# Optimization experiments

Hardware: AMD Instinct MI355X
Metric: run time of the kernel (lower is better)

## Reference

```python
import jax, jax.numpy as jnp
import numpy as np

N_EMBD = 1024
N_HEAD = 16
HEAD_DIM = N_EMBD // N_HEAD


def setup_inputs() -> dict:
    key = jax.random.key(0)
    k1, k2, k3, k4, k5 = jax.random.split(key, 5)
    x = jax.random.normal(k1, (4, 2048, N_EMBD), dtype=jnp.float32)
    s_in = 1.0 / np.sqrt(N_EMBD)
    W_attn = jax.random.normal(k2, (N_EMBD, 3 * N_EMBD), dtype=jnp.float32) * s_in
    b_attn = jax.random.normal(k3, (3 * N_EMBD,), dtype=jnp.float32) * 0.01
    W_proj = jax.random.normal(k4, (N_EMBD, N_EMBD), dtype=jnp.float32) * s_in
    b_proj = jax.random.normal(k5, (N_EMBD,), dtype=jnp.float32) * 0.01
    return {"x": x, "W_attn": W_attn, "b_attn": b_attn, "W_proj": W_proj, "b_proj": b_proj}


def reference(x, W_attn, b_attn, W_proj, b_proj):
    B, T, C = x.shape
    qkv = jnp.einsum('btc,cd->btd', x, W_attn) + b_attn  # [B,T,3C]
    q, k, v = jnp.split(qkv, 3, axis=2)
    # [B,T,C] -> [B,H,T,Dh]
    def heads(t):
        return t.reshape(B, T, N_HEAD, HEAD_DIM).transpose(0, 2, 1, 3)
    q, k, v = heads(q), heads(k), heads(v)
    scale = HEAD_DIM ** -0.5
    att = jnp.einsum('bhqd,bhkd->bhqk', q, k) * scale  # [B,H,T,T]
    causal = jnp.tril(jnp.ones((T, T), dtype=bool))
    att = jnp.where(causal[None, None], att, -jnp.inf)
    att = jax.nn.softmax(att, axis=-1)
    y = jnp.einsum('bhqk,bhkd->bhqd', att, v)  # [B,H,T,Dh]
    y = y.transpose(0, 2, 1, 3).reshape(B, T, C)
    y = jnp.einsum('btc,cd->btd', y, W_proj) + b_proj
    return y
```

## Files before the change

kernel.cpp:

```cpp
#include <hip/hip_runtime.h>

typedef unsigned short u16;
typedef unsigned int u32;
typedef __bf16 bf16x8 __attribute__((ext_vector_type(8)));
typedef u16 u16x8 __attribute__((ext_vector_type(8)));
typedef u16 u16x4 __attribute__((ext_vector_type(4)));
typedef float f32x4 __attribute__((ext_vector_type(4)));
typedef float f32x16 __attribute__((ext_vector_type(16)));

#define BHTD 8388608
#define QSCALE 0.18033688f
#define SMAX 16.0f

__device__ __forceinline__ u16 f2bf(float f) {
  union { float f; u32 u; } x; x.f = f;
  u32 r = (x.u + 0x7FFFu + ((x.u >> 16) & 1u)) >> 16;
  return (u16)r;
}

__device__ __forceinline__ u32 cvt_pk_bf16(float lo, float hi) {
  u32 r;
  asm("v_cvt_pk_bf16_f32 %0, %1, %2" : "=v"(r) : "v"(lo), "v"(hi));
  return r;
}

__device__ __forceinline__ void permlane32_swap(u32& x, u32& y) {
  asm("v_permlane32_swap_b32 %0, %1" : "+v"(x), "+v"(y));
}

__device__ __forceinline__ void async_copy16(const u16* gsrc, u16* ldst) {
  __builtin_amdgcn_global_load_lds(
      (const __attribute__((address_space(1))) void*)gsrc,
      (__attribute__((address_space(3))) void*)ldst, 16, 0, 0);
}

__global__ __launch_bounds__(256) void conv_x_kernel(const float4* __restrict__ in,
                                                     u16x4* __restrict__ out, int n4) {
  int i = blockIdx.x * 256 + threadIdx.x;
  int stride = gridDim.x * 256;
  for (; i < n4; i += stride) {
    float4 v = in[i];
    u16x4 o = { f2bf(v.x), f2bf(v.y), f2bf(v.z), f2bf(v.w) };
    out[i] = o;
  }
}

__global__ __launch_bounds__(256) void transpose_bf16(const float* __restrict__ W,
                                                      u16* __restrict__ Wt, int K, int N) {
  __shared__ float t[64][65];
  int c0 = blockIdx.x * 64;
  int r0 = blockIdx.y * 64;
  int c = threadIdx.x & 63;
  int r4 = threadIdx.x >> 6;
#pragma unroll
  for (int j = 0; j < 16; ++j) {
    int r = j * 4 + r4;
    t[r][c] = W[(size_t)(r0 + r) * N + (c0 + c)];
  }
  __syncthreads();
#pragma unroll
  for (int j = 0; j < 16; ++j) {
    int n = j * 4 + r4;
    Wt[(size_t)(c0 + n) * K + (r0 + c)] = f2bf(t[c][n]);
  }
}

template <int MODE>
__global__ __launch_bounds__(256) void gemm_bf16(const u16* __restrict__ A,
                                                 const u16* __restrict__ Bt,
                                                 const float* __restrict__ bias,
                                                 float* __restrict__ outp,
                                                 u16* __restrict__ qkv, int grid_n) {
  __shared__ __attribute__((aligned(16))) u16 A_lds[128 * 64];
  __shared__ __attribute__((aligned(16))) u16 B_lds[128 * 64];
  const int tid = threadIdx.x;
  const int lane = tid & 63, wave = tid >> 6;
  const int wr = wave >> 1, wc = wave & 1;
  const int bn = blockIdx.x % grid_n, bm = blockIdx.x / grid_n;
  const int m0 = bm * 128, n0 = bn * 128;
  const int g = lane >> 4, c16 = lane & 15;
  const int lrow = lane >> 3, lslot = lane & 7;

  f32x4 acc[4][4] = {};

  for (int kt = 0; kt < 16; ++kt) {
#pragma unroll
    for (int i = 0; i < 4; ++i) {
      int mloc = (wave * 4 + i) * 8 + lrow;
      int col = kt * 64 + ((lslot ^ (mloc & 7)) << 3);
      async_copy16(&A[(size_t)(m0 + mloc) * 1024 + col], &A_lds[(wave * 4 + i) * 512]);
      async_copy16(&Bt[(size_t)(n0 + mloc) * 1024 + col], &B_lds[(wave * 4 + i) * 512]);
    }
    __syncthreads();
#pragma unroll
    for (int kk = 0; kk < 2; ++kk) {
      bf16x8 af[4], bfr[4];
#pragma unroll
      for (int mb = 0; mb < 4; ++mb) {
        int row = wr * 64 + mb * 16 + c16;
        int slot = (kk * 4 + g) ^ (row & 7);
        af[mb] = *(const bf16x8*)&A_lds[row * 64 + slot * 8];
        int rowb = wc * 64 + mb * 16 + c16;
        int slotb = (kk * 4 + g) ^ (rowb & 7);
        bfr[mb] = *(const bf16x8*)&B_lds[rowb * 64 + slotb * 8];
      }
#pragma unroll
      for (int mb = 0; mb < 4; ++mb)
#pragma unroll
        for (int nb = 0; nb < 4; ++nb)
          acc[mb][nb] = __builtin_amdgcn_mfma_f32_16x16x32_bf16(af[mb], bfr[nb], acc[mb][nb], 0, 0, 0);
    }
    __syncthreads();
  }

  float bv[4];
#pragma unroll
  for (int nb = 0; nb < 4; ++nb) bv[nb] = bias[n0 + wc * 64 + nb * 16 + c16];

#pragma unroll
  for (int mb = 0; mb < 4; ++mb) {
    int row0 = m0 + wr * 64 + mb * 16 + g * 4;
#pragma unroll
    for (int nb = 0; nb < 4; ++nb) {
      int col = n0 + wc * 64 + nb * 16 + c16;
      float bvn = bv[nb];
      if (MODE == 0) {
        int sel = col >> 10, ci = col & 1023;
        int hh = ci >> 6, d = ci & 63;
        int bb = row0 >> 11, t0 = row0 & 2047;
        float qs = (sel == 0) ? QSCALE : 1.0f;
        if (sel == 2) {
          u16x4 pk;
#pragma unroll
          for (int r = 0; r < 4; ++r) pk[r] = f2bf(acc[mb][nb][r] + bvn);
          *(u16x4*)&qkv[(size_t)2 * BHTD + (((size_t)(bb * 16 + hh) * 64 + d) << 11) + t0] = pk;
        } else {
#pragma unroll
          for (int r = 0; r < 4; ++r) {
            qkv[(size_t)sel * BHTD + (((size_t)(bb * 16 + hh) * 2048 + t0 + r) << 6) + d] =
                f2bf((acc[mb][nb][r] + bvn) * qs);
          }
        }
      } else {
#pragma unroll
        for (int r = 0; r < 4; ++r)
          outp[((size_t)(row0 + r) << 10) + col] = acc[mb][nb][r] + bvn;
      }
    }
  }
}

__global__ __launch_bounds__(512, 4) void attn_fwd(const u16* __restrict__ Q,
                                                   const u16* __restrict__ K,
                                                   const u16* __restrict__ VT,
                                                   u16* __restrict__ Y) {
  __shared__ __attribute__((aligned(16))) u16 Kl[2][2][64 * 64];
  __shared__ __attribute__((aligned(16))) u16 Vl[2][2][64 * 64];
  float* Pl = (float*)&Kl[0][0][0];
  float* Ll = (float*)&Vl[0][0][0];
  const float NEG_BIG = -1e30f;

  int bid = blockIdx.x;
  int p = bid >> 6, hd = bid & 63;
  size_t hb = (size_t)hd * (2048 * 64);
  const u16* Qh = Q + hb;
  const u16* Kh = K + hb;
  const u16* Vh = VT + hb;
  int tid = threadIdx.x, lane = tid & 63, w = tid >> 6;
  int rg = w & 3, par = w >> 2;
  int c32 = lane & 31, h = lane >> 5;
  const int xs = c32 & 7;

  int srow = tid >> 3;
  int swz = ((tid & 7) ^ (srow & 7)) << 3;

  for (int pass = 0; pass < 2; ++pass) {
    const int t128 = pass ? p : (15 - p);
    const int iters = t128 + 1;
    const int qrow = t128 * 128 + rg * 32 + c32;

    bf16x8 qf[4];
#pragma unroll
    for (int dk = 0; dk < 4; ++dk)
      qf[dk] = *(const bf16x8*)&Qh[(size_t)qrow * 64 + dk * 16 + 8 * h];

    async_copy16(&Kh[(size_t)srow * 64 + swz], &Kl[0][0][tid << 3]);
    async_copy16(&Kh[(size_t)(64 + srow) * 64 + swz], &Kl[0][1][tid << 3]);
    async_copy16(&Vh[(size_t)srow * 2048 + swz], &Vl[0][0][tid << 3]);
    async_copy16(&Vh[(size_t)srow * 2048 + 64 + swz], &Vl[0][1][tid << 3]);

    float l = 0.f;
    f32x16 o0 = {}, o1 = {};

    for (int it = 0; it < iters; ++it) {
      int cb = it & 1;
      __syncthreads();

      if (it + 1 < iters) {
        int kve = (it + 1) << 7, kvo = kve + 64;
        async_copy16(&Kh[(size_t)(kve + srow) * 64 + swz], &Kl[cb ^ 1][0][tid << 3]);
        async_copy16(&Kh[(size_t)(kvo + srow) * 64 + swz], &Kl[cb ^ 1][1][tid << 3]);
        async_copy16(&Vh[(size_t)srow * 2048 + kve + swz], &Vl[cb ^ 1][0][tid << 3]);
        async_copy16(&Vh[(size_t)srow * 2048 + kvo + swz], &Vl[cb ^ 1][1][tid << 3]);
      }

      const bool lastit = (it + 1 == iters);
      if (par && lastit && rg < 2) continue;
      const int kv0 = (2 * it + par) << 6;
      const bool mask = lastit && ((par == 0) == (rg < 2));

      bf16x8 kf[2][4];
#pragma unroll
      for (int kb = 0; kb < 2; ++kb)
#pragma unroll
        for (int dk = 0; dk < 4; ++dk)
          kf[kb][dk] =
              *(const bf16x8*)&Kl[cb][par][(kb * 32 + c32) * 64 + (((2 * dk + h) ^ xs) << 3)];
      f32x16 s0, s1;
#pragma unroll
      for (int i = 0; i < 16; ++i) { s0[i] = -SMAX; s1[i] = -SMAX; }
      __builtin_amdgcn_s_setprio(1);
#pragma unroll
      for (int dk = 0; dk < 4; ++dk) {
        s0 = __builtin_amdgcn_mfma_f32_32x32x16_bf16(kf[0][dk], qf[dk], s0, 0, 0, 0);
        s1 = __builtin_amdgcn_mfma_f32_32x32x16_bf16(kf[1][dk], qf[dk], s1, 0, 0, 0);
      }
      __builtin_amdgcn_s_setprio(0);

      if (mask) {
        int kvb = kv0 + 4 * h;
#pragma unroll
        for (int reg = 0; reg < 16; ++reg) {
          int kvl = kvb + 8 * (reg >> 2) + (reg & 3);
          if (kvl > qrow) s0[reg] = NEG_BIG;
          if (kvl + 32 > qrow) s1[reg] = NEG_BIG;
        }
      }

#pragma unroll
      for (int i = 0; i < 16; ++i) s0[i] = __builtin_exp2f(s0[i]);
#pragma unroll
      for (int i = 0; i < 16; ++i) s1[i] = __builtin_exp2f(s1[i]);
      float b0 = s0[0] + s1[0], b1 = s0[1] + s1[1];
      float b2 = s0[2] + s1[2], b3 = s0[3] + s1[3];
#pragma unroll
      for (int i = 4; i < 16; i += 4) {
        b0 += s0[i] + s1[i];
        b1 += s0[i + 1] + s1[i + 1];
        b2 += s0[i + 2] + s1[i + 2];
        b3 += s0[i + 3] + s1[i + 3];
      }
      float rs = (b0 + b1) + (b2 + b3);
      rs += __shfl_xor(rs, 32);
      l += rs;

      u32 pw0[8], pw1[8];
#pragma unroll
      for (int mm = 0; mm < 8; ++mm) {
        pw0[mm] = cvt_pk_bf16(s0[2 * mm], s0[2 * mm + 1]);
        pw1[mm] = cvt_pk_bf16(s1[2 * mm], s1[2 * mm + 1]);
      }
      permlane32_swap(pw0[0], pw0[2]); permlane32_swap(pw0[1], pw0[3]);
      permlane32_swap(pw0[4], pw0[6]); permlane32_swap(pw0[5], pw0[7]);
      permlane32_swap(pw1[0], pw1[2]); permlane32_swap(pw1[1], pw1[3]);
      permlane32_swap(pw1[4], pw1[6]); permlane32_swap(pw1[5], pw1[7]);

      __builtin_amdgcn_s_setprio(1);
#pragma unroll
      for (int c = 0; c < 4; ++c) {
        const u32* pp = (c >> 1) ? pw1 : pw0;
        const int a = 4 * (c & 1);
        union { u32 u[4]; bf16x8 v; } pf;
        pf.u[0] = pp[a + 0];
        pf.u[1] = pp[a + 1];
        pf.u[2] = pp[a + 2];
        pf.u[3] = pp[a + 3];
        bf16x8 vfa = *(const bf16x8*)&Vl[cb][par][c32 * 64 + (((2 * c + h) ^ xs) << 3)];
        bf16x8 vfb = *(const bf16x8*)&Vl[cb][par][(32 + c32) * 64 + (((2 * c + h) ^ xs) << 3)];
        o0 = __builtin_amdgcn_mfma_f32_32x32x16_bf16(vfa, pf.v, o0, 0, 0, 0);
        o1 = __builtin_amdgcn_mfma_f32_32x32x16_bf16(vfb, pf.v, o1, 0, 0, 0);
      }
      __builtin_amdgcn_s_setprio(0);
    }

    __syncthreads();

    if (par == 1) {
#pragma unroll
      for (int db = 0; db < 2; ++db)
#pragma unroll
        for (int rq = 0; rq < 4; ++rq)
#pragma unroll
          for (int jj = 0; jj < 4; ++jj) {
            int d = db * 32 + 8 * rq + 4 * h + jj;
            Pl[rg * 2048 + d * 32 + c32] = (db ? o1[rq * 4 + jj] : o0[rq * 4 + jj]);
          }
      if (h == 0) Ll[rg * 32 + c32] = l;
    }
    __syncthreads();
    if (par == 0) {
      float lt = l + Ll[rg * 32 + c32];
      float inv = 1.0f / lt;
      size_t yb =
          (size_t)(hd >> 4) * (2048 * 1024) + (size_t)(hd & 15) * 64 + (size_t)qrow * 1024;
#pragma unroll
      for (int db = 0; db < 2; ++db)
#pragma unroll
        for (int rq = 0; rq < 4; ++rq) {
          u16x4 pk;
#pragma unroll
          for (int jj = 0; jj < 4; ++jj) {
            int d = db * 32 + 8 * rq + 4 * h + jj;
            float v = (db ? o1[rq * 4 + jj] : o0[rq * 4 + jj]) + Pl[rg * 2048 + d * 32 + c32];
            pk[jj] = f2bf(v * inv);
          }
          *(u16x4*)&Y[yb + db * 32 + 8 * rq + 4 * h] = pk;
        }
    }
    __syncthreads();
  }
}

extern "C" void kernel_launch(void* const* d_in, const int* in_sizes, int n_in,
                              void* d_out, int out_size, void* d_ws, size_t ws_size,
                              hipStream_t stream) {
  (void)in_sizes; (void)n_in; (void)out_size; (void)ws_size;
  const float* x      = (const float*)d_in[0];
  const float* W_attn = (const float*)d_in[1];
  const float* b_attn = (const float*)d_in[2];
  const float* W_proj = (const float*)d_in[3];
  const float* b_proj = (const float*)d_in[4];
  float* out = (float*)d_out;

  char* ws = (char*)d_ws;
  u16* Xb  = (u16*)(ws);
  u16* Wt  = (u16*)(ws + 16777216);
  u16* Wpt = (u16*)(ws + 16777216 + 6291456);
  u16* QKV = (u16*)(ws + 16777216 + 6291456 + 2097152);
  u16* Yb  = Xb;

  conv_x_kernel<<<2048, 256, 0, stream>>>((const float4*)x, (u16x4*)Xb, 2097152);
  transpose_bf16<<<dim3(48, 16), 256, 0, stream>>>(W_attn, Wt, 1024, 3072);
  transpose_bf16<<<dim3(16, 16), 256, 0, stream>>>(W_proj, Wpt, 1024, 1024);
  gemm_bf16<0><<<1536, 256, 0, stream>>>(Xb, Wt, b_attn, nullptr, QKV, 24);
  attn_fwd<<<512, 512, 0, stream>>>(QKV, QKV + BHTD, QKV + 2 * BHTD, Yb);
  gemm_bf16<1><<<512, 256, 0, stream>>>(Yb, Wpt, b_proj, out, nullptr, 8);
}
```

Measured before the change: 184.4 us.

## Pipeline GEMM with triple-buffered LDS, 256x128 tiles and interleaved MFMA phases

After: 175.6 us. 4.8% less time.

```diff
diff --git a/kernel.cpp b/kernel.cpp
--- a/kernel.cpp
+++ b/kernel.cpp
@@ -33,6 +33,8 @@
       (const __attribute__((address_space(1))) void*)gsrc,
       (__attribute__((address_space(3))) void*)ldst, 16, 0, 0);
 }
+
+#define MF(a, b, c) __builtin_amdgcn_mfma_f32_16x16x32_bf16((a), (b), (c), 0, 0, 0)
 
 __global__ __launch_bounds__(256) void conv_x_kernel(const float4* __restrict__ in,
                                                      u16x4* __restrict__ out, int n4) {
@@ -66,51 +68,128 @@
 }
 
 template <int MODE>
-__global__ __launch_bounds__(256) void gemm_bf16(const u16* __restrict__ A,
-                                                 const u16* __restrict__ Bt,
-                                                 const float* __restrict__ bias,
-                                                 float* __restrict__ outp,
-                                                 u16* __restrict__ qkv, int grid_n) {
-  __shared__ __attribute__((aligned(16))) u16 A_lds[128 * 64];
-  __shared__ __attribute__((aligned(16))) u16 B_lds[128 * 64];
+__global__ __launch_bounds__(512, 2) void gemm_bf16(const u16* __restrict__ A,
+                                                    const u16* __restrict__ Bt,
+                                                    const float* __restrict__ bias,
+                                                    float* __restrict__ outp,
+                                                    u16* __restrict__ qkv, int grid_n) {
+  __shared__ __attribute__((aligned(16))) u16 Al[3][256 * 64];
+  __shared__ __attribute__((aligned(16))) u16 Bl[3][128 * 64];
   const int tid = threadIdx.x;
   const int lane = tid & 63, wave = tid >> 6;
   const int wr = wave >> 1, wc = wave & 1;
   const int bn = blockIdx.x % grid_n, bm = blockIdx.x / grid_n;
-  const int m0 = bm * 128, n0 = bn * 128;
+  const int m0 = bm * 256, n0 = bn * 128;
   const int g = lane >> 4, c16 = lane & 15;
-  const int lrow = lane >> 3, lslot = lane & 7;
+  const int xs = c16 & 7;
+  const int offK0 = ((g ^ xs) << 3);
+  const int offK1 = (((4 + g) ^ xs) << 3);
+
+#define STAGE_A_(t, s, c)                                                         \
+  {                                                                               \
+    int row_ = (c) >> 3, sl_ = (c) & 7;                                           \
+    async_copy16(&A[(size_t)(m0 + row_) * 1024 + (t) * 64 + ((sl_ ^ (row_ & 7)) << 3)], \
+                 &Al[s][(c) << 3]);                                               \
+  }
+#define STAGE_B_(t, s, c)                                                         \
+  {                                                                               \
+    int row_ = (c) >> 3, sl_ = (c) & 7;                                           \
+    async_copy16(&Bt[(size_t)(n0 + row_) * 1024 + (t) * 64 + ((sl_ ^ (row_ & 7)) << 3)], \
+                 &Bl[s][(c) << 3]);                                               \
+  }
 
   f32x4 acc[4][4] = {};
-
-  for (int kt = 0; kt < 16; ++kt) {
-#pragma unroll
-    for (int i = 0; i < 4; ++i) {
-      int mloc = (wave * 4 + i) * 8 + lrow;
-      int col = kt * 64 + ((lslot ^ (mloc & 7)) << 3);
-      async_copy16(&A[(size_t)(m0 + mloc) * 1024 + col], &A_lds[(wave * 4 + i) * 512]);
-      async_copy16(&Bt[(size_t)(n0 + mloc) * 1024 + col], &B_lds[(wave * 4 + i) * 512]);
-    }
-    __syncthreads();
-#pragma unroll
-    for (int kk = 0; kk < 2; ++kk) {
-      bf16x8 af[4], bfr[4];
-#pragma unroll
-      for (int mb = 0; mb < 4; ++mb) {
-        int row = wr * 64 + mb * 16 + c16;
-        int slot = (kk * 4 + g) ^ (row & 7);
-        af[mb] = *(const bf16x8*)&A_lds[row * 64 + slot * 8];
-        int rowb = wc * 64 + mb * 16 + c16;
-        int slotb = (kk * 4 + g) ^ (rowb & 7);
-        bfr[mb] = *(const bf16x8*)&B_lds[rowb * 64 + slotb * 8];
-      }
-#pragma unroll
-      for (int mb = 0; mb < 4; ++mb)
-#pragma unroll
-        for (int nb = 0; nb < 4; ++nb)
-          acc[mb][nb] = __builtin_amdgcn_mfma_f32_16x16x32_bf16(af[mb], bfr[nb], acc[mb][nb], 0, 0, 0);
-    }
-    __syncthreads();
+  bf16x8 aF[2][4][2], bF[2][4][2];
+
+#pragma unroll
+  for (int t = 0; t < 3; ++t) {
+    STAGE_B_(t, t, tid); STAGE_B_(t, t, tid + 512);
+    STAGE_A_(t, t, tid); STAGE_A_(t, t, tid + 512);
+    STAGE_A_(t, t, tid + 1024); STAGE_A_(t, t, tid + 1536);
+  }
+  asm volatile("s_waitcnt vmcnt(12)" ::: "memory");
+  __builtin_amdgcn_s_barrier();
+#pragma unroll
+  for (int m = 0; m < 4; ++m) {
+    int row = wr * 64 + m * 16 + c16;
+    aF[0][m][0] = *(const bf16x8*)&Al[0][row * 64 + offK0];
+    aF[0][m][1] = *(const bf16x8*)&Al[0][row * 64 + offK1];
+  }
+#pragma unroll
+  for (int n = 0; n < 4; ++n) {
+    int row = wc * 64 + n * 16 + c16;
+    bF[0][n][0] = *(const bf16x8*)&Bl[0][row * 64 + offK0];
+    bF[0][n][1] = *(const bf16x8*)&Bl[0][row * 64 + offK1];
+  }
+  asm volatile("s_waitcnt lgkmcnt(0)" ::: "memory");
+  __builtin_amdgcn_s_barrier();
+
+#pragma unroll
+  for (int j = 0; j < 16; ++j) {
+    const int cur = j & 1, nxt = cur ^ 1;
+    const int sR = (j + 1) % 3;
+    const int sW = j % 3;
+    const bool rd = (j < 15);
+    const bool st = (j < 13);
+
+    if (j <= 13) {
+      asm volatile("s_waitcnt vmcnt(6)" ::: "memory");
+    } else if (j == 14) {
+      asm volatile("s_waitcnt vmcnt(0)" ::: "memory");
+    }
+    __builtin_amdgcn_s_barrier();
+
+    if (rd) {
+#pragma unroll
+      for (int m = 0; m < 4; ++m) {
+        int row = wr * 64 + m * 16 + c16;
+        aF[nxt][m][0] = *(const bf16x8*)&Al[sR][row * 64 + offK0];
+        aF[nxt][m][1] = *(const bf16x8*)&Al[sR][row * 64 + offK1];
+      }
+    }
+    if (st) STAGE_B_(j + 3, sW, tid);
+    __builtin_amdgcn_s_setprio(1);
+#pragma unroll
+    for (int n = 0; n < 4; ++n) acc[0][n] = MF(aF[cur][0][0], bF[cur][n][0], acc[0][n]);
+#pragma unroll
+    for (int n = 0; n < 4; ++n) acc[1][n] = MF(aF[cur][1][0], bF[cur][n][0], acc[1][n]);
+    __builtin_amdgcn_s_setprio(0);
+    __builtin_amdgcn_s_barrier();
+
+    if (rd) {
+#pragma unroll
+      for (int n = 0; n < 4; ++n) {
+        int row = wc * 64 + n * 16 + c16;
+        bF[nxt][n][0] = *(const bf16x8*)&Bl[sR][row * 64 + offK0];
+        bF[nxt][n][1] = *(const bf16x8*)&Bl[sR][row * 64 + offK1];
+      }
+    }
+    if (st) STAGE_B_(j + 3, sW, tid + 512);
+    __builtin_amdgcn_s_setprio(1);
+#pragma unroll
+    for (int n = 0; n < 4; ++n) acc[2][n] = MF(aF[cur][2][0], bF[cur][n][0], acc[2][n]);
+#pragma unroll
+    for (int n = 0; n < 4; ++n) acc[3][n] = MF(aF[cur][3][0], bF[cur][n][0], acc[3][n]);
+    __builtin_amdgcn_s_setprio(0);
+    __builtin_amdgcn_s_barrier();
+
+    if (st) { STAGE_A_(j + 3, sW, tid); STAGE_A_(j + 3, sW, tid + 512); }
+    __builtin_amdgcn_s_setprio(1);
+#pragma unroll
+    for (int n = 0; n < 4; ++n) acc[0][n] = MF(aF[cur][0][1], bF[cur][n][1], acc[0][n]);
+#pragma unroll
+    for (int n = 0; n < 4; ++n) acc[1][n] = MF(aF[cur][1][1], bF[cur][n][1], acc[1][n]);
+    __builtin_amdgcn_s_setprio(0);
+    __builtin_amdgcn_s_barrier();
+
+    if (st) { STAGE_A_(j + 3, sW, tid + 1024); STAGE_A_(j + 3, sW, tid + 1536); }
+    __builtin_amdgcn_s_setprio(1);
+#pragma unroll
+    for (int n = 0; n < 4; ++n) acc[2][n] = MF(aF[cur][2][1], bF[cur][n][1], acc[2][n]);
+#pragma unroll
+    for (int n = 0; n < 4; ++n) acc[3][n] = MF(aF[cur][3][1], bF[cur][n][1], acc[3][n]);
+    __builtin_amdgcn_s_setprio(0);
+    __builtin_amdgcn_s_barrier();
   }
 
   float bv[4];
@@ -148,6 +227,8 @@
       }
     }
   }
+#undef STAGE_A_
+#undef STAGE_B_
 }
 
 __global__ __launch_bounds__(512, 4) void attn_fwd(const u16* __restrict__ Q,
@@ -342,7 +423,7 @@
   conv_x_kernel<<<2048, 256, 0, stream>>>((const float4*)x, (u16x4*)Xb, 2097152);
   transpose_bf16<<<dim3(48, 16), 256, 0, stream>>>(W_attn, Wt, 1024, 3072);
   transpose_bf16<<<dim3(16, 16), 256, 0, stream>>>(W_proj, Wpt, 1024, 1024);
-  gemm_bf16<0><<<1536, 256, 0, stream>>>(Xb, Wt, b_attn, nullptr, QKV, 24);
+  gemm_bf16<0><<<768, 512, 0, stream>>>(Xb, Wt, b_attn, nullptr, QKV, 24);
   attn_fwd<<<512, 512, 0, stream>>>(QKV, QKV + BHTD, QKV + 2 * BHTD, Yb);
-  gemm_bf16<1><<<512, 256, 0, stream>>>(Yb, Wpt, b_proj, out, nullptr, 8);
-}
+  gemm_bf16<1><<<256, 512, 0, stream>>>(Yb, Wpt, b_proj, out, nullptr, 8);
+}
```
